# Kernel tuning notes

Measured on AMD Instinct MI355X. Metric: run time of the kernel, lower is better.

The kernel has to match this reference:

```python
import jax, jax.numpy as jnp
import numpy as np

FORGET_BIAS = 1.0

def _lstm_step(c, h, x, W, b):
    # TF BasicLSTMCell: concat([x, h]) @ W + b -> split into i, j, f, o
    gates = jnp.concatenate([x, h], axis=-1) @ W + b
    i, j, f, o = jnp.split(gates, 4, axis=-1)
    new_c = c * jax.nn.sigmoid(f + FORGET_BIAS) + jax.nn.sigmoid(i) * jnp.tanh(j)
    new_h = jnp.tanh(new_c) * jax.nn.sigmoid(o)
    return new_c, new_h

def setup_inputs() -> dict:
    key = jax.random.key(0)
    ks = jax.random.split(key, 8)
    B, T, D, H, C = 64, 128, 2048, 512, 101
    s1 = 1.0 / np.sqrt(D + H)
    s2 = 1.0 / np.sqrt(2 * H)
    so = 1.0 / np.sqrt(H)
    return {
        "inputs": jax.random.normal(ks[0], (B, T, D), dtype=jnp.float32),
        "labels": jax.random.randint(ks[1], (B, T), 0, C, dtype=jnp.int64),
        "W1": jax.random.normal(ks[2], (D + H, 4 * H), dtype=jnp.float32) * s1,
        "b1": jnp.zeros((4 * H,), dtype=jnp.float32),
        "W2": jax.random.normal(ks[3], (2 * H, 4 * H), dtype=jnp.float32) * s2,
        "b2": jnp.zeros((4 * H,), dtype=jnp.float32),
        "Wout": jax.random.normal(ks[4], (H, C), dtype=jnp.float32) * so,
        "bout": jnp.zeros((C,), dtype=jnp.float32),
    }

def reference(inputs, labels, W1, b1, W2, b2, Wout, bout):
    B, T, D = inputs.shape
    H = Wout.shape[0]

    def step(carry, x_t):
        (c1, h1), (c2, h2) = carry
        c1, h1 = _lstm_step(c1, h1, x_t, W1, b1)
        c2, h2 = _lstm_step(c2, h2, h1, W2, b2)
        return ((c1, h1), (c2, h2)), h2

    zeros = jnp.zeros((B, H), dtype=inputs.dtype)
    init = ((zeros, zeros), (zeros, zeros))
    xs = jnp.swapaxes(inputs, 0, 1)  # [T, B, D]
    _, hs = jax.lax.scan(step, init, xs)  # hs: [T, B, H]
    outputs = jnp.swapaxes(hs, 0, 1)  # [B, T, H]

    logits = outputs @ Wout + bout  # [B, T, C]
    preds = jax.nn.softmax(logits, axis=-1)
    log_probs = jax.nn.log_softmax(logits, axis=-1)
    ce = -jnp.take_along_axis(log_probs, labels[..., None], axis=-1)[..., 0]  # [B, T]
    cost = jnp.mean(jnp.sum(ce, axis=1))
    return preds, cost
```

## Files before the change

### kernel.cpp

```cpp
#include <hip/hip_runtime.h>
#include <cmath>

#define Bb   64
#define Tt   128
#define Dd   2048
#define Hh   512
#define Gg   2048
#define Cc   101
#define PC   112
#define ROWS 8192

typedef unsigned short u16;
typedef __attribute__((ext_vector_type(8))) short bf16x8;
typedef __attribute__((ext_vector_type(4))) float f32x4;

__device__ __forceinline__ u16 bf16rne(float x) {
  unsigned u = __float_as_uint(x);
  unsigned r = (u + 0x7fffu + ((u >> 16) & 1u)) >> 16;
  return (u16)r;
}
__device__ __forceinline__ void split_bf16(float x, u16& h, u16& l) {
  h = bf16rne(x);
  l = bf16rne(x - __uint_as_float(((unsigned)h) << 16));
}
__device__ __forceinline__ float sigm(float x) { return 1.f / (1.f + expf(-x)); }

__global__ __launch_bounds__(256)
void convert_hilo(const float* __restrict__ src, u16* __restrict__ hi,
                  u16* __restrict__ lo, int n4) {
  for (int i = blockIdx.x * 256 + threadIdx.x; i < n4; i += gridDim.x * 256) {
    const float4 v = ((const float4*)src)[i];
    ushort4 h, l;
    split_bf16(v.x, h.x, l.x);
    split_bf16(v.y, h.y, l.y);
    split_bf16(v.z, h.z, l.z);
    split_bf16(v.w, h.w, l.w);
    ((ushort4*)hi)[i] = h;
    ((ushort4*)lo)[i] = l;
  }
}

__global__ __launch_bounds__(256)
void convertT_w1(const float* __restrict__ W1, u16* __restrict__ Th,
                 u16* __restrict__ Tl) {
  __shared__ float tl[32][33];
  const int tx = threadIdx.x, ty = threadIdx.y;
  const int k0 = blockIdx.x * 32, c0 = blockIdx.y * 32;
#pragma unroll
  for (int j = 0; j < 4; ++j)
    tl[ty + j * 8][tx] = W1[(size_t)(k0 + ty + j * 8) * Gg + (c0 + tx)];
  __syncthreads();
#pragma unroll
  for (int j = 0; j < 4; ++j) {
    const float v = tl[tx][ty + j * 8];
    u16 h, l;
    split_bf16(v, h, l);
    const size_t o = (size_t)(c0 + ty + j * 8) * Dd + (k0 + tx);
    Th[o] = h;
    Tl[o] = l;
  }
}

__global__ __launch_bounds__(256)
void convert_woutT(const float* __restrict__ Wout, u16* __restrict__ Th,
                   u16* __restrict__ Tl) {
  const int c = blockIdx.x;
  for (int k = threadIdx.x; k < Hh; k += 256) {
    const float v = (c < Cc) ? Wout[k * Cc + c] : 0.f;
    u16 h, l;
    split_bf16(v, h, l);
    Th[c * Hh + k] = h;
    Tl[c * Hh + k] = l;
  }
}

__global__ __launch_bounds__(256)
void permuteW(const float* __restrict__ src, u16* __restrict__ dh,
              u16* __restrict__ dl, int K) {
  __shared__ float tl[32][33];
  const int tx = threadIdx.x, ty = threadIdx.y;
  const int k0 = blockIdx.x * 32, c0 = blockIdx.y * 32;
#pragma unroll
  for (int j = 0; j < 4; ++j)
    tl[ty + j * 8][tx] = src[(size_t)(k0 + ty + j * 8) * Gg + (c0 + tx)];
  __syncthreads();
#pragma unroll
  for (int j = 0; j < 4; ++j) {
    const int col = c0 + ty + j * 8;
    const int g = col >> 9, mg = col & 511;
    const int cg = mg >> 2, m = mg & 3;
    const float v = tl[tx][ty + j * 8];
    u16 h, l;
    split_bf16(v, h, l);
    const size_t o = (size_t)(cg * 16 + g * 4 + m) * K + k0 + tx;
    dh[o] = h;
    dl[o] = l;
  }
}

__global__ __launch_bounds__(256)
void gemm1_mfma(const u16* __restrict__ Ah, const u16* __restrict__ Al,
                const u16* __restrict__ Bh, const u16* __restrict__ Bl,
                const float* __restrict__ bias, float* __restrict__ C) {
  __shared__ u16 Ash[128][40];
  __shared__ u16 Asl[128][40];
  __shared__ u16 Bsh[128][40];
  __shared__ u16 Bsl[128][40];
  const int tid  = threadIdx.x;
  const int lane = tid & 63, wave = tid >> 6;
  const int wm = wave >> 1, wn = wave & 1;
  const int l15 = lane & 15, k8 = (lane >> 4) * 8, r4 = (lane >> 4) * 4;
  const int row0 = blockIdx.y * 128, col0 = blockIdx.x * 128;
  const int srow = tid >> 1, sk = (tid & 1) * 16;

  const u16* pAh = Ah + (size_t)(row0 + srow) * Dd + sk;
  const u16* pAl = Al + (size_t)(row0 + srow) * Dd + sk;
  const u16* pBh = Bh + (size_t)(col0 + srow) * Dd + sk;
  const u16* pBl = Bl + (size_t)(col0 + srow) * Dd + sk;

  f32x4 acc[4][4];
#pragma unroll
  for (int i = 0; i < 4; ++i)
#pragma unroll
    for (int j = 0; j < 4; ++j) acc[i][j] = (f32x4){0.f, 0.f, 0.f, 0.f};

  for (int k0 = 0; k0 < Dd; k0 += 32) {
    *(bf16x8*)(&Ash[srow][sk])     = *(const bf16x8*)(pAh + k0);
    *(bf16x8*)(&Ash[srow][sk + 8]) = *(const bf16x8*)(pAh + k0 + 8);
    *(bf16x8*)(&Asl[srow][sk])     = *(const bf16x8*)(pAl + k0);
    *(bf16x8*)(&Asl[srow][sk + 8]) = *(const bf16x8*)(pAl + k0 + 8);
    *(bf16x8*)(&Bsh[srow][sk])     = *(const bf16x8*)(pBh + k0);
    *(bf16x8*)(&Bsh[srow][sk + 8]) = *(const bf16x8*)(pBh + k0 + 8);
    *(bf16x8*)(&Bsl[srow][sk])     = *(const bf16x8*)(pBl + k0);
    *(bf16x8*)(&Bsl[srow][sk + 8]) = *(const bf16x8*)(pBl + k0 + 8);
    __syncthreads();

    bf16x8 afh[4], afl[4], bfh[4], bfl[4];
#pragma unroll
    for (int mt = 0; mt < 4; ++mt) {
      afh[mt] = *(const bf16x8*)(&Ash[wm * 64 + mt * 16 + l15][k8]);
      afl[mt] = *(const bf16x8*)(&Asl[wm * 64 + mt * 16 + l15][k8]);
    }
#pragma unroll
    for (int nt = 0; nt < 4; ++nt) {
      bfh[nt] = *(const bf16x8*)(&Bsh[wn * 64 + nt * 16 + l15][k8]);
      bfl[nt] = *(const bf16x8*)(&Bsl[wn * 64 + nt * 16 + l15][k8]);
    }
#pragma unroll
    for (int mt = 0; mt < 4; ++mt)
#pragma unroll
      for (int nt = 0; nt < 4; ++nt) {
        acc[mt][nt] = __builtin_amdgcn_mfma_f32_16x16x32_bf16(
            afh[mt], bfh[nt], acc[mt][nt], 0, 0, 0);
        acc[mt][nt] = __builtin_amdgcn_mfma_f32_16x16x32_bf16(
            afh[mt], bfl[nt], acc[mt][nt], 0, 0, 0);
        acc[mt][nt] = __builtin_amdgcn_mfma_f32_16x16x32_bf16(
            afl[mt], bfh[nt], acc[mt][nt], 0, 0, 0);
      }
    __syncthreads();
  }

#pragma unroll
  for (int nt = 0; nt < 4; ++nt) {
    const int col = col0 + wn * 64 + nt * 16 + l15;
    const float bj = bias[col];
#pragma unroll
    for (int mt = 0; mt < 4; ++mt) {
      float* Cp = C + (size_t)(row0 + wm * 64 + mt * 16 + r4) * Gg + col;
#pragma unroll
      for (int r = 0; r < 4; ++r)
        Cp[(size_t)r * Gg] = acc[mt][nt][r] + bj;
    }
  }
}

__global__ __launch_bounds__(256)
void gemm_proj(const u16* __restrict__ Ah, const u16* __restrict__ Al,
               const u16* __restrict__ Bh, const u16* __restrict__ Bl,
               const float* __restrict__ bout, float* __restrict__ logits) {
  __shared__ u16 Ash[128][40];
  __shared__ u16 Asl[128][40];
  __shared__ u16 Bsh[PC][40];
  __shared__ u16 Bsl[PC][40];
  const int tid  = threadIdx.x;
  const int lane = tid & 63, wave = tid >> 6;
  const int l15 = lane & 15, k8 = (lane >> 4) * 8, r4 = (lane >> 4) * 4;
  const int row0 = blockIdx.x * 128;
  const int srow = tid >> 1, sk = (tid & 1) * 16;

  const u16* pAh = Ah + (size_t)(row0 + srow) * Hh + sk;
  const u16* pAl = Al + (size_t)(row0 + srow) * Hh + sk;
  const u16* pBh = Bh + (size_t)srow * Hh + sk;
  const u16* pBl = Bl + (size_t)srow * Hh + sk;

  f32x4 acc[2][7];
#pragma unroll
  for (int i = 0; i < 2; ++i)
#pragma unroll
    for (int j = 0; j < 7; ++j) acc[i][j] = (f32x4){0.f, 0.f, 0.f, 0.f};

  for (int k0 = 0; k0 < Hh; k0 += 32) {
    *(bf16x8*)(&Ash[srow][sk])     = *(const bf16x8*)(pAh + k0);
    *(bf16x8*)(&Ash[srow][sk + 8]) = *(const bf16x8*)(pAh + k0 + 8);
    *(bf16x8*)(&Asl[srow][sk])     = *(const bf16x8*)(pAl + k0);
    *(bf16x8*)(&Asl[srow][sk + 8]) = *(const bf16x8*)(pAl + k0 + 8);
    if (srow < PC) {
      *(bf16x8*)(&Bsh[srow][sk])     = *(const bf16x8*)(pBh + k0);
      *(bf16x8*)(&Bsh[srow][sk + 8]) = *(const bf16x8*)(pBh + k0 + 8);
      *(bf16x8*)(&Bsl[srow][sk])     = *(const bf16x8*)(pBl + k0);
      *(bf16x8*)(&Bsl[srow][sk + 8]) = *(const bf16x8*)(pBl + k0 + 8);
    }
    __syncthreads();

    bf16x8 afh[2], afl[2], bfh[7], bfl[7];
#pragma unroll
    for (int mt = 0; mt < 2; ++mt) {
      afh[mt] = *(const bf16x8*)(&Ash[wave * 32 + mt * 16 + l15][k8]);
      afl[mt] = *(const bf16x8*)(&Asl[wave * 32 + mt * 16 + l15][k8]);
    }
#pragma unroll
    for (int nt = 0; nt < 7; ++nt) {
      bfh[nt] = *(const bf16x8*)(&Bsh[nt * 16 + l15][k8]);
      bfl[nt] = *(const bf16x8*)(&Bsl[nt * 16 + l15][k8]);
    }
#pragma unroll
    for (int mt = 0; mt < 2; ++mt)
#pragma unroll
      for (int nt = 0; nt < 7; ++nt) {
        acc[mt][nt] = __builtin_amdgcn_mfma_f32_16x16x32_bf16(
            afh[mt], bfh[nt], acc[mt][nt], 0, 0, 0);
        acc[mt][nt] = __builtin_amdgcn_mfma_f32_16x16x32_bf16(
            afh[mt], bfl[nt], acc[mt][nt], 0, 0, 0);
        acc[mt][nt] = __builtin_amdgcn_mfma_f32_16x16x32_bf16(
            afl[mt], bfh[nt], acc[mt][nt], 0, 0, 0);
      }
    __syncthreads();
  }

#pragma unroll
  for (int nt = 0; nt < 7; ++nt) {
    const int col = nt * 16 + l15;
    const float bj = (col < Cc) ? bout[col] : 0.f;
#pragma unroll
    for (int mt = 0; mt < 2; ++mt) {
      float* Lp = logits + (size_t)(row0 + wave * 32 + mt * 16 + r4) * PC + col;
#pragma unroll
      for (int r = 0; r < 4; ++r)
        Lp[(size_t)r * PC] = acc[mt][nt][r] + bj;
    }
  }
}

__global__ __launch_bounds__(256)
void softmax_ce(const float* __restrict__ logits, const int* __restrict__ labels,
                float* __restrict__ preds, float* __restrict__ ce) {
  const int lane = threadIdx.x & 63, wv = threadIdx.x >> 6;
  const int row = blockIdx.x * 4 + wv;
  const float* lg = logits + (size_t)row * PC;
  const bool a0 = (lane < Cc), a1 = (lane + 64 < Cc);
  const float v0 = a0 ? lg[lane] : -INFINITY;
  const float v1 = a1 ? lg[lane + 64] : -INFINITY;
  float m = fmaxf(v0, v1);
#pragma unroll
  for (int off = 32; off > 0; off >>= 1) m = fmaxf(m, __shfl_xor(m, off));
  const float e0 = a0 ? expf(v0 - m) : 0.f;
  const float e1 = a1 ? expf(v1 - m) : 0.f;
  float s = e0 + e1;
#pragma unroll
  for (int off = 32; off > 0; off >>= 1) s += __shfl_xor(s, off);
  if (a0) preds[(size_t)row * Cc + lane] = e0 / s;
  if (a1) preds[(size_t)row * Cc + lane + 64] = e1 / s;
  const int lab = labels[row];
  if (lab == lane)           ce[row] = logf(s) + m - v0;
  else if (lab == lane + 64) ce[row] = logf(s) + m - v1;
}

#define BM 128
#define BN 128
#define BK 16

__global__ __launch_bounds__(256)
void sgemm_bias(const float* __restrict__ A, const float* __restrict__ B,
                const float* __restrict__ bias, float* __restrict__ C,
                int M, int N, int K) {
  __shared__ float As[BK][BM];
  __shared__ float Bs[BK][BN];
  const int tid  = threadIdx.x;
  const int row0 = blockIdx.y * BM, col0 = blockIdx.x * BN;
  const int tr = (tid >> 4) << 3;
  const int tc = (tid & 15) << 3;

  float acc[8][8];
#pragma unroll
  for (int i = 0; i < 8; ++i)
#pragma unroll
    for (int j = 0; j < 8; ++j) acc[i][j] = 0.f;

  const int arow = tid >> 1;
  const int acol = (tid & 1) << 3;
  const int brow = tid >> 4;
  const int bcol = (tid & 15) << 3;
  const float* Ap = A + (size_t)(row0 + arow) * K + acol;
  const float* Bp = B + (size_t)brow * N + (col0 + bcol);

  for (int k0 = 0; k0 < K; k0 += BK) {
    const float4 a0 = *(const float4*)(Ap + k0);
    const float4 a1 = *(const float4*)(Ap + k0 + 4);
    const float4 bv0 = *(const float4*)(Bp + (size_t)k0 * N);
    const float4 bv1 = *(const float4*)(Bp + (size_t)k0 * N + 4);
    As[acol + 0][arow] = a0.x;
    As[acol + 1][arow] = a0.y;
    As[acol + 2][arow] = a0.z;
    As[acol + 3][arow] = a0.w;
    As[acol + 4][arow] = a1.x;
    As[acol + 5][arow] = a1.y;
    As[acol + 6][arow] = a1.z;
    As[acol + 7][arow] = a1.w;
    *(float4*)(&Bs[brow][bcol])     = bv0;
    *(float4*)(&Bs[brow][bcol + 4]) = bv1;
    __syncthreads();
#pragma unroll
    for (int k = 0; k < BK; ++k) {
      float a[8], b[8];
      *(float4*)(a)     = *(const float4*)(&As[k][tr]);
      *(float4*)(a + 4) = *(const float4*)(&As[k][tr + 4]);
      *(float4*)(b)     = *(const float4*)(&Bs[k][tc]);
      *(float4*)(b + 4) = *(const float4*)(&Bs[k][tc + 4]);
#pragma unroll
      for (int i = 0; i < 8; ++i)
#pragma unroll
        for (int j = 0; j < 8; ++j)
          acc[i][j] = fmaf(a[i], b[j], acc[i][j]);
    }
    __syncthreads();
  }

  float bj[8];
#pragma unroll
  for (int j = 0; j < 8; ++j) bj[j] = bias[col0 + tc + j];
#pragma unroll
  for (int i = 0; i < 8; ++i) {
    float* Cp = C + (size_t)(row0 + tr + i) * N + (col0 + tc);
    float4 o0, o1;
    o0.x = acc[i][0] + bj[0]; o0.y = acc[i][1] + bj[1];
    o0.z = acc[i][2] + bj[2]; o0.w = acc[i][3] + bj[3];
    o1.x = acc[i][4] + bj[4]; o1.y = acc[i][5] + bj[5];
    o1.z = acc[i][6] + bj[6]; o1.w = acc[i][7] + bj[7];
    *(float4*)(Cp)     = o0;
    *(float4*)(Cp + 4) = o1;
  }
}

__device__ __forceinline__ void mm_half(
    const u16* __restrict__ hh_src, const u16* __restrict__ hl_src,
    const u16* __restrict__ wph, const u16* __restrict__ wpl, int Kw,
    f32x4& acc, u16 (*Ah)[64][136], u16 (*Al)[64][136],
    u16 (*Bh)[16][136], u16 (*Bl)[16][136], int tid, int lane, int w) {
  const int hr = tid >> 2, hk = (tid & 3) * 32;
  const int wv = tid >> 4, wk = (tid & 15) * 8;
  const int fr = lane & 15, f8 = (lane >> 4) * 8;

  bf16x8 rh[4], rl[4], rwh, rwl;
#pragma unroll
  for (int j = 0; j < 4; ++j) {
    rh[j] = *(const bf16x8*)(hh_src + hr * 512 + hk + j * 8);
    rl[j] = *(const bf16x8*)(hl_src + hr * 512 + hk + j * 8);
  }
  rwh = *(const bf16x8*)(wph + (size_t)wv * Kw + wk);
  rwl = *(const bf16x8*)(wpl + (size_t)wv * Kw + wk);
#pragma unroll
  for (int j = 0; j < 4; ++j) {
    *(bf16x8*)&Ah[0][hr][hk + j * 8] = rh[j];
    *(bf16x8*)&Al[0][hr][hk + j * 8] = rl[j];
  }
  *(bf16x8*)&Bh[0][wv][wk] = rwh;
  *(bf16x8*)&Bl[0][wv][wk] = rwl;
  __syncthreads();

  for (int kc = 0; kc < 4; ++kc) {
    const int cur = kc & 1;
    if (kc < 3) {
      const int ko = (kc + 1) * 128;
#pragma unroll
      for (int j = 0; j < 4; ++j) {
        rh[j] = *(const bf16x8*)(hh_src + hr * 512 + ko + hk + j * 8);
        rl[j] = *(const bf16x8*)(hl_src + hr * 512 + ko + hk + j * 8);
      }
      rwh = *(const bf16x8*)(wph + (size_t)wv * Kw + ko + wk);
      rwl = *(const bf16x8*)(wpl + (size_t)wv * Kw + ko + wk);
    }
#pragma unroll
    for (int s = 0; s < 4; ++s) {
      const bf16x8 afh = *(const bf16x8*)&Ah[cur][w * 16 + fr][s * 32 + f8];
      const bf16x8 afl = *(const bf16x8*)&Al[cur][w * 16 + fr][s * 32 + f8];
      const bf16x8 bfh = *(const bf16x8*)&Bh[cur][fr][s * 32 + f8];
      const bf16x8 bfl = *(const bf16x8*)&Bl[cur][fr][s * 32 + f8];
      acc = __builtin_amdgcn_mfma_f32_16x16x32_bf16(afh, bfh, acc, 0, 0, 0);
      acc = __builtin_amdgcn_mfma_f32_16x16x32_bf16(afh, bfl, acc, 0, 0, 0);
      acc = __builtin_amdgcn_mfma_f32_16x16x32_bf16(afl, bfh, acc, 0, 0, 0);
    }
    if (kc < 3) {
      const int nb = cur ^ 1;
#pragma unroll
      for (int j = 0; j < 4; ++j) {
        *(bf16x8*)&Ah[nb][hr][hk + j * 8] = rh[j];
        *(bf16x8*)&Al[nb][hr][hk + j * 8] = rl[j];
      }
      *(bf16x8*)&Bh[nb][wv][wk] = rwh;
      *(bf16x8*)&Bl[nb][wv][wk] = rwl;
    }
    __syncthreads();
  }
}

__global__ __launch_bounds__(256, 1)
void fused_step2(const float* __restrict__ pre,
                 const u16* __restrict__ WP1h, const u16* __restrict__ WP1l,
                 const u16* __restrict__ WP2h, const u16* __restrict__ WP2l,
                 const float* __restrict__ b2,
                 u16* __restrict__ h1hi, u16* __restrict__ h1lo,
                 u16* __restrict__ h2hi, u16* __restrict__ h2lo,
                 u16* __restrict__ h2fh, u16* __restrict__ h2fl,
                 float* __restrict__ c1, float* __restrict__ c2, int t) {
  __shared__ u16 Ah[2][64][136], Al[2][64][136];
  __shared__ u16 Bh[2][16][136], Bl[2][16][136];
  __shared__ float ex[4][16][17];
  const int tid = threadIdx.x;
  const int lane = tid & 63, w = tid >> 6;
  const int fr = lane & 15;
  const bool isL2 = blockIdx.x >= 128;
  const int cg = blockIdx.x & 127;

  f32x4 acc = {0.f, 0.f, 0.f, 0.f};
  bool have = false;

  if (!isL2) {
    if (t >= Tt) return;
    if (t > 0) {
      const int sl = (t - 1) & 1;
      mm_half(h1hi + (sl << 15), h1lo + (sl << 15),
              WP1h + (size_t)cg * 16 * 512, WP1l + (size_t)cg * 16 * 512, 512,
              acc, Ah, Al, Bh, Bl, tid, lane, w);
      have = true;
    }
  } else {
    if (t < 1) return;
    const u16* A1h = h1hi + (((t - 1) & 1) << 15);
    const u16* A1l = h1lo + (((t - 1) & 1) << 15);
    const u16* A2h = h2hi + (((t - 2) & 1) << 15);
    const u16* A2l = h2lo + (((t - 2) & 1) << 15);
    const u16* ph = WP2h + (size_t)cg * 16 * 1024;
    const u16* pl = WP2l + (size_t)cg * 16 * 1024;
    const bool h2ok = (t >= 2);

    const int hr = tid >> 2, hk = (tid & 3) * 32;
    const int wv = tid >> 4, wk = (tid & 15) * 8;
    const int f8 = (lane >> 4) * 8;

    bf16x8 rh[4], rl[4], rwh, rwl;
#pragma unroll
    for (int j = 0; j < 4; ++j) {
      rh[j] = *(const bf16x8*)(A1h + hr * 512 + hk + j * 8);
      rl[j] = *(const bf16x8*)(A1l + hr * 512 + hk + j * 8);
    }
    rwh = *(const bf16x8*)(ph + (size_t)wv * 1024 + wk);
    rwl = *(const bf16x8*)(pl + (size_t)wv * 1024 + wk);
#pragma unroll
    for (int j = 0; j < 4; ++j) {
      *(bf16x8*)&Ah[0][hr][hk + j * 8] = rh[j];
      *(bf16x8*)&Al[0][hr][hk + j * 8] = rl[j];
    }
    *(bf16x8*)&Bh[0][wv][wk] = rwh;
    *(bf16x8*)&Bl[0][wv][wk] = rwl;
    __syncthreads();

    for (int kc = 0; kc < 8; ++kc) {
      const int cur = kc & 1;
      if (kc < 7) {
        const int nk = kc + 1;
        const u16* sh = (nk < 4) ? A1h : A2h;
        const u16* sl2 = (nk < 4) ? A1l : A2l;
        const int ko = (nk & 3) * 128;
#pragma unroll
        for (int j = 0; j < 4; ++j) {
          rh[j] = *(const bf16x8*)(sh + hr * 512 + ko + hk + j * 8);
          rl[j] = *(const bf16x8*)(sl2 + hr * 512 + ko + hk + j * 8);
        }
        rwh = *(const bf16x8*)(ph + (size_t)wv * 1024 + nk * 128 + wk);
        rwl = *(const bf16x8*)(pl + (size_t)wv * 1024 + nk * 128 + wk);
      }
      if (kc < 4 || h2ok) {
#pragma unroll
        for (int s = 0; s < 4; ++s) {
          const bf16x8 afh = *(const bf16x8*)&Ah[cur][w * 16 + fr][s * 32 + f8];
          const bf16x8 afl = *(const bf16x8*)&Al[cur][w * 16 + fr][s * 32 + f8];
          const bf16x8 bfh = *(const bf16x8*)&Bh[cur][fr][s * 32 + f8];
          const bf16x8 bfl = *(const bf16x8*)&Bl[cur][fr][s * 32 + f8];
          acc = __builtin_amdgcn_mfma_f32_16x16x32_bf16(afh, bfh, acc, 0, 0, 0);
          acc = __builtin_amdgcn_mfma_f32_16x16x32_bf16(afh, bfl, acc, 0, 0, 0);
          acc = __builtin_amdgcn_mfma_f32_16x16x32_bf16(afl, bfh, acc, 0, 0, 0);
        }
      }
      if (kc < 7) {
        const int nb = cur ^ 1;
#pragma unroll
        for (int j = 0; j < 4; ++j) {
          *(bf16x8*)&Ah[nb][hr][hk + j * 8] = rh[j];
          *(bf16x8*)&Al[nb][hr][hk + j * 8] = rl[j];
        }
        *(bf16x8*)&Bh[nb][wv][wk] = rwh;
        *(bf16x8*)&Bl[nb][wv][wk] = rwl;
      }
      __syncthreads();
    }
    have = true;
  }

  if (have) {
#pragma unroll
    for (int r = 0; r < 4; ++r)
      ex[w][(lane >> 4) * 4 + r][fr] = acc[r];
  }
  __syncthreads();

  const int b = tid >> 2, m = tid & 3;
  float s0 = 0.f, s1 = 0.f, s2 = 0.f, s3 = 0.f;
  if (have) {
    s0 = ex[b >> 4][b & 15][0 + m];
    s1 = ex[b >> 4][b & 15][4 + m];
    s2 = ex[b >> 4][b & 15][8 + m];
    s3 = ex[b >> 4][b & 15][12 + m];
  }
  const int col = cg * 4 + m;
  const int ci = b * Hh + col;
  if (!isL2) {
    const float* pp = pre + ((size_t)b * Tt + t) * Gg + col;
    const float gi = pp[0] + s0, gj = pp[512] + s1;
    const float gf = pp[1024] + s2, go = pp[1536] + s3;
    const float cp = (t > 0) ? c1[ci] : 0.f;
    const float nc = fmaf(cp, sigm(gf + 1.f), sigm(gi) * tanhf(gj));
    c1[ci] = nc;
    const float nh = tanhf(nc) * sigm(go);
    u16 hh, hl;
    split_bf16(nh, hh, hl);
    const int hidx = ((t & 1) << 15) + ci;
    h1hi[hidx] = hh;
    h1lo[hidx] = hl;
  } else {
    const float gi = b2[col] + s0, gj = b2[512 + col] + s1;
    const float gf = b2[1024 + col] + s2, go = b2[1536 + col] + s3;
    const float cp = (t >= 2) ? c2[ci] : 0.f;
    const float nc = fmaf(cp, sigm(gf + 1.f), sigm(gi) * tanhf(gj));
    c2[ci] = nc;
    const float nh = tanhf(nc) * sigm(go);
    u16 hh, hl;
    split_bf16(nh, hh, hl);
    const int hidx = (((t - 1) & 1) << 15) + ci;
    h2hi[hidx] = hh;
    h2lo[hidx] = hl;
    const size_t fo = ((size_t)b * Tt + (t - 1)) * Hh + col;
    h2fh[fo] = hh;
    h2fl[fo] = hl;
  }
}

__global__ __launch_bounds__(256)
void reduce_cost(const float* __restrict__ ce, float* __restrict__ out) {
  __shared__ float red[256];
  const int tid = threadIdx.x;
  float s = 0.f;
  for (int i = tid; i < ROWS; i += 256) s += ce[i];
  red[tid] = s;
  __syncthreads();
  for (int st = 128; st > 0; st >>= 1) {
    if (tid < st) red[tid] += red[tid + st];
    __syncthreads();
  }
  if (tid == 0) out[0] = red[0] / (float)Bb;
}

extern "C" void kernel_launch(void* const* d_in, const int* in_sizes, int n_in,
                              void* d_out, int out_size, void* d_ws, size_t ws_size,
                              hipStream_t stream) {
  const float* inputs = (const float*)d_in[0];
  const int*   labels = (const int*)d_in[1];
  const float* W1     = (const float*)d_in[2];
  const float* b1     = (const float*)d_in[3];
  const float* W2     = (const float*)d_in[4];
  const float* b2     = (const float*)d_in[5];
  const float* Wout   = (const float*)d_in[6];
  const float* bout   = (const float*)d_in[7];
  float* out = (float*)d_out;

  float* ws     = (float*)d_ws;
  float* pre    = ws;
  float* c1     = pre    + (size_t)ROWS * Gg;
  float* c2     = c1     + (size_t)Bb * Hh;
  float* ceb    = c2     + (size_t)Bb * Hh;
  float* logits = ceb    + ROWS;
  u16* h1hi = (u16*)(logits + (size_t)ROWS * PC);
  u16* h1lo = h1hi + 2 * 64 * 512;
  u16* h2hi = h1lo + 2 * 64 * 512;
  u16* h2lo = h2hi + 2 * 64 * 512;
  u16* h2fh = h2lo + 2 * 64 * 512;
  u16* h2fl = h2fh + (size_t)ROWS * Hh;
  u16* WP1h = h2fl + (size_t)ROWS * Hh;
  u16* WP1l = WP1h + 128 * 16 * 512;
  u16* WP2h = WP1l + 128 * 16 * 512;
  u16* WP2l = WP2h + 128 * 16 * 1024;
  u16* WoTh = WP2l + 128 * 16 * 1024;
  u16* WoTl = WoTh + PC * Hh;
  u16* Xhi  = WoTl + PC * Hh;
  u16* Xlo  = Xhi  + (size_t)ROWS * Dd;
  u16* W1Th = Xlo  + (size_t)ROWS * Dd;
  u16* W1Tl = W1Th + (size_t)Gg * Dd;
  const size_t need = (size_t)((char*)(W1Tl + (size_t)Gg * Dd) - (char*)d_ws);
  const bool use_mfma = ws_size >= need;

  permuteW<<<dim3(16, 64), dim3(32, 8), 0, stream>>>(
      W1 + (size_t)Dd * Gg, WP1h, WP1l, 512);
  permuteW<<<dim3(32, 64), dim3(32, 8), 0, stream>>>(W2, WP2h, WP2l, 1024);
  convert_woutT<<<PC, 256, 0, stream>>>(Wout, WoTh, WoTl);

  if (use_mfma) {
    convert_hilo<<<2048, 256, 0, stream>>>(inputs, Xhi, Xlo, ROWS * Dd / 4);
    convertT_w1<<<dim3(64, 64), dim3(32, 8), 0, stream>>>(W1, W1Th, W1Tl);
    gemm1_mfma<<<dim3(Gg / 128, ROWS / 128), 256, 0, stream>>>(
        Xhi, Xlo, W1Th, W1Tl, b1, pre);
  } else {
    sgemm_bias<<<dim3(Gg / BN, ROWS / BM), dim3(256), 0, stream>>>(
        inputs, W1, b1, pre, ROWS, Gg, Dd);
  }

  for (int t = 0; t <= Tt; ++t)
    fused_step2<<<256, 256, 0, stream>>>(pre, WP1h, WP1l, WP2h, WP2l, b2,
                                         h1hi, h1lo, h2hi, h2lo,
                                         h2fh, h2fl, c1, c2, t);

  gemm_proj<<<ROWS / 128, 256, 0, stream>>>(h2fh, h2fl, WoTh, WoTl, bout, logits);
  softmax_ce<<<ROWS / 4, 256, 0, stream>>>(logits, labels, out, ceb);
  reduce_cost<<<1, 256, 0, stream>>>(ceb, out + (size_t)ROWS * Cc);
}
```

Measured before the change: 1.783 ms.

## Split recurrent step over batch halves and K-halves across 512 blocks

The per-timestep fused LSTM kernel now launches 512 blocks instead of 256. Each block handles 32 batch rows rather than 64. Within a block, the four waves split into two batch tiles times two K-halves, and the partial sums are reduced through shared memory. The pre-activation loads are hoisted ahead of the matmul, and launch bounds allow two blocks per CU. The goal is more parallelism and lower latency per step in the latency-bound recurrence, at the cost of reading each weight tile twice and an extra shared-memory reduction.

```diff
diff --git a/kernel.cpp b/kernel.cpp
--- a/kernel.cpp
+++ b/kernel.cpp
@@ -351,70 +351,8 @@
   }
 }
 
-__device__ __forceinline__ void mm_half(
-    const u16* __restrict__ hh_src, const u16* __restrict__ hl_src,
-    const u16* __restrict__ wph, const u16* __restrict__ wpl, int Kw,
-    f32x4& acc, u16 (*Ah)[64][136], u16 (*Al)[64][136],
-    u16 (*Bh)[16][136], u16 (*Bl)[16][136], int tid, int lane, int w) {
-  const int hr = tid >> 2, hk = (tid & 3) * 32;
-  const int wv = tid >> 4, wk = (tid & 15) * 8;
-  const int fr = lane & 15, f8 = (lane >> 4) * 8;
-
-  bf16x8 rh[4], rl[4], rwh, rwl;
-#pragma unroll
-  for (int j = 0; j < 4; ++j) {
-    rh[j] = *(const bf16x8*)(hh_src + hr * 512 + hk + j * 8);
-    rl[j] = *(const bf16x8*)(hl_src + hr * 512 + hk + j * 8);
-  }
-  rwh = *(const bf16x8*)(wph + (size_t)wv * Kw + wk);
-  rwl = *(const bf16x8*)(wpl + (size_t)wv * Kw + wk);
-#pragma unroll
-  for (int j = 0; j < 4; ++j) {
-    *(bf16x8*)&Ah[0][hr][hk + j * 8] = rh[j];
-    *(bf16x8*)&Al[0][hr][hk + j * 8] = rl[j];
-  }
-  *(bf16x8*)&Bh[0][wv][wk] = rwh;
-  *(bf16x8*)&Bl[0][wv][wk] = rwl;
-  __syncthreads();
-
-  for (int kc = 0; kc < 4; ++kc) {
-    const int cur = kc & 1;
-    if (kc < 3) {
-      const int ko = (kc + 1) * 128;
-#pragma unroll
-      for (int j = 0; j < 4; ++j) {
-        rh[j] = *(const bf16x8*)(hh_src + hr * 512 + ko + hk + j * 8);
-        rl[j] = *(const bf16x8*)(hl_src + hr * 512 + ko + hk + j * 8);
-      }
-      rwh = *(const bf16x8*)(wph + (size_t)wv * Kw + ko + wk);
-      rwl = *(const bf16x8*)(wpl + (size_t)wv * Kw + ko + wk);
-    }
-#pragma unroll
-    for (int s = 0; s < 4; ++s) {
-      const bf16x8 afh = *(const bf16x8*)&Ah[cur][w * 16 + fr][s * 32 + f8];
-      const bf16x8 afl = *(const bf16x8*)&Al[cur][w * 16 + fr][s * 32 + f8];
-      const bf16x8 bfh = *(const bf16x8*)&Bh[cur][fr][s * 32 + f8];
-      const bf16x8 bfl = *(const bf16x8*)&Bl[cur][fr][s * 32 + f8];
-      acc = __builtin_amdgcn_mfma_f32_16x16x32_bf16(afh, bfh, acc, 0, 0, 0);
-      acc = __builtin_amdgcn_mfma_f32_16x16x32_bf16(afh, bfl, acc, 0, 0, 0);
-      acc = __builtin_amdgcn_mfma_f32_16x16x32_bf16(afl, bfh, acc, 0, 0, 0);
-    }
-    if (kc < 3) {
-      const int nb = cur ^ 1;
-#pragma unroll
-      for (int j = 0; j < 4; ++j) {
-        *(bf16x8*)&Ah[nb][hr][hk + j * 8] = rh[j];
-        *(bf16x8*)&Al[nb][hr][hk + j * 8] = rl[j];
-      }
-      *(bf16x8*)&Bh[nb][wv][wk] = rwh;
-      *(bf16x8*)&Bl[nb][wv][wk] = rwl;
-    }
-    __syncthreads();
-  }
-}
-
-__global__ __launch_bounds__(256, 1)
-void fused_step2(const float* __restrict__ pre,
+__global__ __launch_bounds__(256, 2)
+void fused_step3(const float* __restrict__ pre,
                  const u16* __restrict__ WP1h, const u16* __restrict__ WP1l,
                  const u16* __restrict__ WP2h, const u16* __restrict__ WP2l,
                  const float* __restrict__ b2,
@@ -422,80 +360,119 @@
                  u16* __restrict__ h2hi, u16* __restrict__ h2lo,
                  u16* __restrict__ h2fh, u16* __restrict__ h2fl,
                  float* __restrict__ c1, float* __restrict__ c2, int t) {
-  __shared__ u16 Ah[2][64][136], Al[2][64][136];
+  __shared__ u16 Ah[2][32][136], Al[2][32][136];
   __shared__ u16 Bh[2][16][136], Bl[2][16][136];
-  __shared__ float ex[4][16][17];
+  __shared__ float ex[2][2][16][17];
   const int tid = threadIdx.x;
   const int lane = tid & 63, w = tid >> 6;
-  const int fr = lane & 15;
-  const bool isL2 = blockIdx.x >= 128;
-  const int cg = blockIdx.x & 127;
+  const int bt = w & 1, kh = w >> 1;
+  const int fr = lane & 15, f8 = (lane >> 4) * 8, r4 = (lane >> 4) * 4;
+  const bool isL2 = blockIdx.x >= 256;
+  const int idx = blockIdx.x & 255;
+  const int cg = idx & 127, bg = idx >> 7;
+  const int b0 = bg * 32;
+
+  const int hr = tid >> 3, hk = (tid & 7) * 16;
+  const int wv = tid >> 4, wk = (tid & 15) * 8;
 
   f32x4 acc = {0.f, 0.f, 0.f, 0.f};
   bool have = false;
+  float p0 = 0.f, p1 = 0.f, p2 = 0.f, p3 = 0.f;
+
+  const int eb = tid >> 2, em = tid & 3;
+  const int col = cg * 4 + em;
+  const int ci = (b0 + eb) * Hh + col;
 
   if (!isL2) {
     if (t >= Tt) return;
+    if (tid < 128) {
+      const float* pp = pre + ((size_t)(b0 + eb) * Tt + t) * Gg + col;
+      p0 = pp[0]; p1 = pp[512]; p2 = pp[1024]; p3 = pp[1536];
+    }
     if (t > 0) {
       const int sl = (t - 1) & 1;
-      mm_half(h1hi + (sl << 15), h1lo + (sl << 15),
-              WP1h + (size_t)cg * 16 * 512, WP1l + (size_t)cg * 16 * 512, 512,
-              acc, Ah, Al, Bh, Bl, tid, lane, w);
+      const u16* A_h = h1hi + (sl << 15) + (b0 + hr) * 512 + hk;
+      const u16* A_l = h1lo + (sl << 15) + (b0 + hr) * 512 + hk;
+      const u16* B_h = WP1h + (size_t)(cg * 16 + wv) * 512 + wk;
+      const u16* B_l = WP1l + (size_t)(cg * 16 + wv) * 512 + wk;
+
+      bf16x8 ra0, ra1, rl0, rl1, rwh, rwl;
+      ra0 = *(const bf16x8*)(A_h);     ra1 = *(const bf16x8*)(A_h + 8);
+      rl0 = *(const bf16x8*)(A_l);     rl1 = *(const bf16x8*)(A_l + 8);
+      rwh = *(const bf16x8*)(B_h);     rwl = *(const bf16x8*)(B_l);
+      *(bf16x8*)&Ah[0][hr][hk] = ra0;  *(bf16x8*)&Ah[0][hr][hk + 8] = ra1;
+      *(bf16x8*)&Al[0][hr][hk] = rl0;  *(bf16x8*)&Al[0][hr][hk + 8] = rl1;
+      *(bf16x8*)&Bh[0][wv][wk] = rwh;  *(bf16x8*)&Bl[0][wv][wk] = rwl;
+      __syncthreads();
+
+      for (int kc = 0; kc < 4; ++kc) {
+        const int cur = kc & 1;
+        if (kc < 3) {
+          const int ko = (kc + 1) * 128;
+          ra0 = *(const bf16x8*)(A_h + ko);     ra1 = *(const bf16x8*)(A_h + ko + 8);
+          rl0 = *(const bf16x8*)(A_l + ko);     rl1 = *(const bf16x8*)(A_l + ko + 8);
+          rwh = *(const bf16x8*)(B_h + ko);     rwl = *(const bf16x8*)(B_l + ko);
+        }
+#pragma unroll
+        for (int s = 0; s < 2; ++s) {
+          const int c0 = kh * 64 + s * 32 + f8;
+          const bf16x8 afh = *(const bf16x8*)&Ah[cur][bt * 16 + fr][c0];
+          const bf16x8 afl = *(const bf16x8*)&Al[cur][bt * 16 + fr][c0];
+          const bf16x8 bfh = *(const bf16x8*)&Bh[cur][fr][c0];
+          const bf16x8 bfl = *(const bf16x8*)&Bl[cur][fr][c0];
+          acc = __builtin_amdgcn_mfma_f32_16x16x32_bf16(afh, bfh, acc, 0, 0, 0);
+          acc = __builtin_amdgcn_mfma_f32_16x16x32_bf16(afh, bfl, acc, 0, 0, 0);
+          acc = __builtin_amdgcn_mfma_f32_16x16x32_bf16(afl, bfh, acc, 0, 0, 0);
+        }
+        if (kc < 3) {
+          const int nb = cur ^ 1;
+          *(bf16x8*)&Ah[nb][hr][hk] = ra0;  *(bf16x8*)&Ah[nb][hr][hk + 8] = ra1;
+          *(bf16x8*)&Al[nb][hr][hk] = rl0;  *(bf16x8*)&Al[nb][hr][hk + 8] = rl1;
+          *(bf16x8*)&Bh[nb][wv][wk] = rwh;  *(bf16x8*)&Bl[nb][wv][wk] = rwl;
+        }
+        __syncthreads();
+      }
       have = true;
     }
   } else {
     if (t < 1) return;
-    const u16* A1h = h1hi + (((t - 1) & 1) << 15);
-    const u16* A1l = h1lo + (((t - 1) & 1) << 15);
-    const u16* A2h = h2hi + (((t - 2) & 1) << 15);
-    const u16* A2l = h2lo + (((t - 2) & 1) << 15);
-    const u16* ph = WP2h + (size_t)cg * 16 * 1024;
-    const u16* pl = WP2l + (size_t)cg * 16 * 1024;
+    const u16* A1h = h1hi + (((t - 1) & 1) << 15) + (b0 + hr) * 512 + hk;
+    const u16* A1l = h1lo + (((t - 1) & 1) << 15) + (b0 + hr) * 512 + hk;
+    const u16* A2h = h2hi + (((t - 2) & 1) << 15) + (b0 + hr) * 512 + hk;
+    const u16* A2l = h2lo + (((t - 2) & 1) << 15) + (b0 + hr) * 512 + hk;
+    const u16* B_h = WP2h + (size_t)(cg * 16 + wv) * 1024 + wk;
+    const u16* B_l = WP2l + (size_t)(cg * 16 + wv) * 1024 + wk;
     const bool h2ok = (t >= 2);
 
-    const int hr = tid >> 2, hk = (tid & 3) * 32;
-    const int wv = tid >> 4, wk = (tid & 15) * 8;
-    const int f8 = (lane >> 4) * 8;
-
-    bf16x8 rh[4], rl[4], rwh, rwl;
-#pragma unroll
-    for (int j = 0; j < 4; ++j) {
-      rh[j] = *(const bf16x8*)(A1h + hr * 512 + hk + j * 8);
-      rl[j] = *(const bf16x8*)(A1l + hr * 512 + hk + j * 8);
-    }
-    rwh = *(const bf16x8*)(ph + (size_t)wv * 1024 + wk);
-    rwl = *(const bf16x8*)(pl + (size_t)wv * 1024 + wk);
-#pragma unroll
-    for (int j = 0; j < 4; ++j) {
-      *(bf16x8*)&Ah[0][hr][hk + j * 8] = rh[j];
-      *(bf16x8*)&Al[0][hr][hk + j * 8] = rl[j];
-    }
-    *(bf16x8*)&Bh[0][wv][wk] = rwh;
-    *(bf16x8*)&Bl[0][wv][wk] = rwl;
+    bf16x8 ra0, ra1, rl0, rl1, rwh, rwl;
+    ra0 = *(const bf16x8*)(A1h);     ra1 = *(const bf16x8*)(A1h + 8);
+    rl0 = *(const bf16x8*)(A1l);     rl1 = *(const bf16x8*)(A1l + 8);
+    rwh = *(const bf16x8*)(B_h);     rwl = *(const bf16x8*)(B_l);
+    *(bf16x8*)&Ah[0][hr][hk] = ra0;  *(bf16x8*)&Ah[0][hr][hk + 8] = ra1;
+    *(bf16x8*)&Al[0][hr][hk] = rl0;  *(bf16x8*)&Al[0][hr][hk + 8] = rl1;
+    *(bf16x8*)&Bh[0][wv][wk] = rwh;  *(bf16x8*)&Bl[0][wv][wk] = rwl;
     __syncthreads();
 
     for (int kc = 0; kc < 8; ++kc) {
       const int cur = kc & 1;
       if (kc < 7) {
         const int nk = kc + 1;
-        const u16* sh = (nk < 4) ? A1h : A2h;
+        const u16* sh  = (nk < 4) ? A1h : A2h;
         const u16* sl2 = (nk < 4) ? A1l : A2l;
         const int ko = (nk & 3) * 128;
-#pragma unroll
-        for (int j = 0; j < 4; ++j) {
-          rh[j] = *(const bf16x8*)(sh + hr * 512 + ko + hk + j * 8);
-          rl[j] = *(const bf16x8*)(sl2 + hr * 512 + ko + hk + j * 8);
-        }
-        rwh = *(const bf16x8*)(ph + (size_t)wv * 1024 + nk * 128 + wk);
-        rwl = *(const bf16x8*)(pl + (size_t)wv * 1024 + nk * 128 + wk);
+        ra0 = *(const bf16x8*)(sh + ko);      ra1 = *(const bf16x8*)(sh + ko + 8);
+        rl0 = *(const bf16x8*)(sl2 + ko);     rl1 = *(const bf16x8*)(sl2 + ko + 8);
+        rwh = *(const bf16x8*)(B_h + nk * 128);
+        rwl = *(const bf16x8*)(B_l + nk * 128);
       }
       if (kc < 4 || h2ok) {
 #pragma unroll
-        for (int s = 0; s < 4; ++s) {
-          const bf16x8 afh = *(const bf16x8*)&Ah[cur][w * 16 + fr][s * 32 + f8];
-          const bf16x8 afl = *(const bf16x8*)&Al[cur][w * 16 + fr][s * 32 + f8];
-          const bf16x8 bfh = *(const bf16x8*)&Bh[cur][fr][s * 32 + f8];
-          const bf16x8 bfl = *(const bf16x8*)&Bl[cur][fr][s * 32 + f8];
+        for (int s = 0; s < 2; ++s) {
+          const int c0 = kh * 64 + s * 32 + f8;
+          const bf16x8 afh = *(const bf16x8*)&Ah[cur][bt * 16 + fr][c0];
+          const bf16x8 afl = *(const bf16x8*)&Al[cur][bt * 16 + fr][c0];
+          const bf16x8 bfh = *(const bf16x8*)&Bh[cur][fr][c0];
+          const bf16x8 bfl = *(const bf16x8*)&Bl[cur][fr][c0];
           acc = __builtin_amdgcn_mfma_f32_16x16x32_bf16(afh, bfh, acc, 0, 0, 0);
           acc = __builtin_amdgcn_mfma_f32_16x16x32_bf16(afh, bfl, acc, 0, 0, 0);
           acc = __builtin_amdgcn_mfma_f32_16x16x32_bf16(afl, bfh, acc, 0, 0, 0);
@@ -503,13 +480,9 @@
       }
       if (kc < 7) {
         const int nb = cur ^ 1;
-#pragma unroll
-        for (int j = 0; j < 4; ++j) {
-          *(bf16x8*)&Ah[nb][hr][hk + j * 8] = rh[j];
-          *(bf16x8*)&Al[nb][hr][hk + j * 8] = rl[j];
-        }
-        *(bf16x8*)&Bh[nb][wv][wk] = rwh;
-        *(bf16x8*)&Bl[nb][wv][wk] = rwl;
+        *(bf16x8*)&Ah[nb][hr][hk] = ra0;  *(bf16x8*)&Ah[nb][hr][hk + 8] = ra1;
+        *(bf16x8*)&Al[nb][hr][hk] = rl0;  *(bf16x8*)&Al[nb][hr][hk + 8] = rl1;
+        *(bf16x8*)&Bh[nb][wv][wk] = rwh;  *(bf16x8*)&Bl[nb][wv][wk] = rwl;
       }
       __syncthreads();
     }
@@ -519,48 +492,46 @@
   if (have) {
 #pragma unroll
     for (int r = 0; r < 4; ++r)
-      ex[w][(lane >> 4) * 4 + r][fr] = acc[r];
+      ex[kh][bt][r4 + r][fr] = acc[r];
   }
   __syncthreads();
 
-  const int b = tid >> 2, m = tid & 3;
-  float s0 = 0.f, s1 = 0.f, s2 = 0.f, s3 = 0.f;
-  if (have) {
-    s0 = ex[b >> 4][b & 15][0 + m];
-    s1 = ex[b >> 4][b & 15][4 + m];
-    s2 = ex[b >> 4][b & 15][8 + m];
-    s3 = ex[b >> 4][b & 15][12 + m];
-  }
-  const int col = cg * 4 + m;
-  const int ci = b * Hh + col;
-  if (!isL2) {
-    const float* pp = pre + ((size_t)b * Tt + t) * Gg + col;
-    const float gi = pp[0] + s0, gj = pp[512] + s1;
-    const float gf = pp[1024] + s2, go = pp[1536] + s3;
-    const float cp = (t > 0) ? c1[ci] : 0.f;
-    const float nc = fmaf(cp, sigm(gf + 1.f), sigm(gi) * tanhf(gj));
-    c1[ci] = nc;
-    const float nh = tanhf(nc) * sigm(go);
-    u16 hh, hl;
-    split_bf16(nh, hh, hl);
-    const int hidx = ((t & 1) << 15) + ci;
-    h1hi[hidx] = hh;
-    h1lo[hidx] = hl;
-  } else {
-    const float gi = b2[col] + s0, gj = b2[512 + col] + s1;
-    const float gf = b2[1024 + col] + s2, go = b2[1536 + col] + s3;
-    const float cp = (t >= 2) ? c2[ci] : 0.f;
-    const float nc = fmaf(cp, sigm(gf + 1.f), sigm(gi) * tanhf(gj));
-    c2[ci] = nc;
-    const float nh = tanhf(nc) * sigm(go);
-    u16 hh, hl;
-    split_bf16(nh, hh, hl);
-    const int hidx = (((t - 1) & 1) << 15) + ci;
-    h2hi[hidx] = hh;
-    h2lo[hidx] = hl;
-    const size_t fo = ((size_t)b * Tt + (t - 1)) * Hh + col;
-    h2fh[fo] = hh;
-    h2fl[fo] = hl;
+  if (tid < 128) {
+    const int bte = eb >> 4, bl = eb & 15;
+    float s0 = 0.f, s1 = 0.f, s2 = 0.f, s3 = 0.f;
+    if (have) {
+      s0 = ex[0][bte][bl][0 + em] + ex[1][bte][bl][0 + em];
+      s1 = ex[0][bte][bl][4 + em] + ex[1][bte][bl][4 + em];
+      s2 = ex[0][bte][bl][8 + em] + ex[1][bte][bl][8 + em];
+      s3 = ex[0][bte][bl][12 + em] + ex[1][bte][bl][12 + em];
+    }
+    if (!isL2) {
+      const float gi = p0 + s0, gj = p1 + s1, gf = p2 + s2, go = p3 + s3;
+      const float cp = (t > 0) ? c1[ci] : 0.f;
+      const float nc = fmaf(cp, sigm(gf + 1.f), sigm(gi) * tanhf(gj));
+      c1[ci] = nc;
+      const float nh = tanhf(nc) * sigm(go);
+      u16 hh, hl;
+      split_bf16(nh, hh, hl);
+      const int hidx = ((t & 1) << 15) + ci;
+      h1hi[hidx] = hh;
+      h1lo[hidx] = hl;
+    } else {
+      const float gi = b2[col] + s0, gj = b2[512 + col] + s1;
+      const float gf = b2[1024 + col] + s2, go = b2[1536 + col] + s3;
+      const float cp = (t >= 2) ? c2[ci] : 0.f;
+      const float nc = fmaf(cp, sigm(gf + 1.f), sigm(gi) * tanhf(gj));
+      c2[ci] = nc;
+      const float nh = tanhf(nc) * sigm(go);
+      u16 hh, hl;
+      split_bf16(nh, hh, hl);
+      const int hidx = (((t - 1) & 1) << 15) + ci;
+      h2hi[hidx] = hh;
+      h2lo[hidx] = hl;
+      const size_t fo = ((size_t)(b0 + eb) * Tt + (t - 1)) * Hh + col;
+      h2fh[fo] = hh;
+      h2fl[fo] = hl;
+    }
   }
 }
 
@@ -633,7 +604,7 @@
   }
 
   for (int t = 0; t <= Tt; ++t)
-    fused_step2<<<256, 256, 0, stream>>>(pre, WP1h, WP1l, WP2h, WP2l, b2,
+    fused_step3<<<512, 256, 0, stream>>>(pre, WP1h, WP1l, WP2h, WP2l, b2,
                                          h1hi, h1lo, h2hi, h2lo,
                                          h2fh, h2fl, c1, c2, t);
 
```

New measurement: 1.529 ms. 14.3% less time.
